# Kernel tuning notes

Hardware: AMD Instinct MI355X
Metric: run time of the kernel (lower is better)

## Reference

```python
import jax, jax.numpy as jnp
import numpy as np

# Production-scale dims: ViT patch attention on a 32x32 patch grid
B, L, F = 16, 1024, 512      # batch, seq (=NX*NY patches), model dim
H, D = 8, 64                 # heads, head_dim (F = H*D)
NX, NY = 32, 32              # patch grid; Toeplitz table size 4*NX*NY = 4096


def setup_inputs() -> dict:
    key = jax.random.key(0)
    ks = jax.random.split(key, 12)
    w = lambda k, shp: jax.random.normal(k, shp, jnp.float32) * 0.02
    return {
        "inputs_q": jax.random.normal(ks[0], (B, L, F), jnp.float32),
        "inputs_kv": jax.random.normal(ks[1], (B, L, F), jnp.float32),
        "Wq": w(ks[2], (F, H * D)), "bq": jnp.zeros((H * D,), jnp.float32),
        "Wk": w(ks[3], (F, H * D)), "bk": jnp.zeros((H * D,), jnp.float32),
        "Wv": w(ks[4], (F, H * D)), "bv": jnp.zeros((H * D,), jnp.float32),
        "Wo": w(ks[5], (H * D, F)), "bo": jnp.zeros((F,), jnp.float32),
        "toeplitz": w(ks[6], (H, 4 * NX * NY)),
    }


def _rel_index():
    # 2D relative-position (Toeplitz) index: patch p -> (x, y) on NX x NY grid.
    coords = jnp.arange(L)
    xi, yi = coords // NY, coords % NY
    dx = xi[:, None] - xi[None, :] + NX          # in [1, 2*NX-1]
    dy = yi[:, None] - yi[None, :] + NY          # in [1, 2*NY-1]
    return dx * (2 * NY) + dy                    # [L, L] indices into 4*NX*NY table


def reference(inputs_q, inputs_kv, Wq, bq, Wk, bk, Wv, bv, Wo, bo, toeplitz):
    q = (inputs_q @ Wq + bq).reshape(B, L, H, D)
    k = (inputs_kv @ Wk + bk).reshape(B, L, H, D)
    v = (inputs_kv @ Wv + bv).reshape(B, L, H, D)
    bias = toeplitz[:, _rel_index()]             # [H, L, L] Toeplitz relative bias
    scale = 1.0 / jnp.sqrt(jnp.float32(D))
    scores = jnp.einsum("bqhd,bkhd->bhqk", q, k) * scale + bias  # [B,H,L,L]
    attn = jax.nn.softmax(scores, axis=-1)
    x = jnp.einsum("bhqk,bkhd->bqhd", attn, v).reshape(B, L, H * D)
    out = x @ Wo + bo
    return out.reshape(B, L, H, D)               # matches torch forward's final reshape
```

## Files before the change

### kernel.cpp

```cpp
#include <hip/hip_runtime.h>
#include <hip/hip_bf16.h>

#define B_  16
#define L_  1024
#define F_  512
#define H_  8
#define D_  64
#define M_  (B_ * L_)
#define HD_ 512

typedef __bf16 bf16x8 __attribute__((ext_vector_type(8)));
typedef __bf16 bf16x4 __attribute__((ext_vector_type(4)));
typedef short  s16x4  __attribute__((ext_vector_type(4)));
typedef float  f32x4  __attribute__((ext_vector_type(4)));

__device__ __forceinline__ void gl_lds16(const void* g, void* l) {
  __builtin_amdgcn_global_load_lds(
      (const __attribute__((address_space(1))) unsigned int*)g,
      (__attribute__((address_space(3))) unsigned int*)l, 16, 0, 0);
}

__device__ __forceinline__ float exp2_fast(float x) {
  float r;
  asm("v_exp_f32 %0, %1" : "=v"(r) : "v"(x));
  return r;
}

#define WAIT_VM_LG(N)                                                           \
  asm volatile("s_waitcnt vmcnt(" #N ") lgkmcnt(0)" ::: "memory")
#define BARRIER() asm volatile("s_barrier" ::: "memory")

#define QSCALE 0.18033688f
#define LOG2E  1.44269504f

__global__ __launch_bounds__(256) void wt_kernel(
    const float* __restrict__ Wq, const float* __restrict__ Wk,
    const float* __restrict__ Wv, const float* __restrict__ Wo,
    __bf16* __restrict__ Wt_all)
{
  const float* W = (blockIdx.z == 0) ? Wq : (blockIdx.z == 1) ? Wk
                 : (blockIdx.z == 2) ? Wv : Wo;
  __bf16* Wt = Wt_all + (size_t)blockIdx.z * (512 * 512);
  __shared__ float s[32][33];
  const int t = threadIdx.x;
  const int r = t >> 5, c = t & 31;
  const int k0 = blockIdx.x * 32, n0 = blockIdx.y * 32;
#pragma unroll
  for (int i = 0; i < 4; ++i)
    s[r + i * 8][c] = W[(size_t)(k0 + r + i * 8) * 512 + n0 + c];
  __syncthreads();
#pragma unroll
  for (int i = 0; i < 4; ++i)
    Wt[(size_t)(n0 + r + i * 8) * 512 + k0 + c] = (__bf16)s[c][r + i * 8];
}

__global__ __launch_bounds__(256) void gemm_proj_kernel(
    const float* __restrict__ Xq, const float* __restrict__ Xkv,
    const __bf16* __restrict__ Wt_all,
    const float* __restrict__ bq, const float* __restrict__ bk_,
    const float* __restrict__ bv_,
    __bf16* __restrict__ qd, __bf16* __restrict__ kd, __bf16* __restrict__ vd)
{
  const int by = blockIdx.y;
  const int seg = by >> 2;
  const float* X = (seg == 0) ? Xq : Xkv;
  const __bf16* Wt = Wt_all + (size_t)seg * 262144;
  const float* bias = (seg == 0) ? bq : (seg == 1) ? bk_ : bv_;
  __bf16* dst = (seg == 0) ? qd : (seg == 1) ? kd : vd;
  const int mode = seg;
  const float oscale = (seg == 0) ? QSCALE : 1.0f;

  __shared__ __align__(16) __bf16 As[2][4][128][8];
  __shared__ __align__(16) __bf16 Bs[3][4][128][8];
  const int t = threadIdx.x;
  const int m0 = blockIdx.x * 128, n0 = (by & 3) * 128;
  const int lane = t & 63, w = t >> 6;
  const int ml = lane & 15, quad = lane >> 4;
  const int wm = w & 1, wn = w >> 1;

  f32x4 acc[4][4];
#pragma unroll
  for (int i = 0; i < 4; ++i)
#pragma unroll
    for (int j = 0; j < 4; ++j) acc[i][j] = (f32x4){0.f, 0.f, 0.f, 0.f};

  const int ako0 = t & 3,          arow0 = t >> 2;
  const int ako1 = (t + 256) & 3,  arow1 = (t + 256) >> 2;
  const int bs0 = w * 64 + lane,   bs1 = (w + 4) * 64 + lane;
  const int bko0 = bs0 >> 7, brow0 = bs0 & 127;
  const int bko1 = bs1 >> 7, brow1 = bs1 & 127;

  float4 fa0, fa1, fa2, fa3;

#define ALOAD(kk)                                                               \
  do {                                                                          \
    const float* p0 = X + (size_t)(m0 + arow0) * 512 + (kk) + ako0 * 8;         \
    const float* p1 = X + (size_t)(m0 + arow1) * 512 + (kk) + ako1 * 8;         \
    fa0 = *(const float4*)p0; fa1 = *(const float4*)(p0 + 4);                   \
    fa2 = *(const float4*)p1; fa3 = *(const float4*)(p1 + 4);                   \
  } while (0)

#define AWRITE(buf)                                                             \
  do {                                                                          \
    bf16x8 v0, v1;                                                              \
    v0[0] = (__bf16)fa0.x; v0[1] = (__bf16)fa0.y; v0[2] = (__bf16)fa0.z;        \
    v0[3] = (__bf16)fa0.w; v0[4] = (__bf16)fa1.x; v0[5] = (__bf16)fa1.y;        \
    v0[6] = (__bf16)fa1.z; v0[7] = (__bf16)fa1.w;                               \
    v1[0] = (__bf16)fa2.x; v1[1] = (__bf16)fa2.y; v1[2] = (__bf16)fa2.z;        \
    v1[3] = (__bf16)fa2.w; v1[4] = (__bf16)fa3.x; v1[5] = (__bf16)fa3.y;        \
    v1[6] = (__bf16)fa3.z; v1[7] = (__bf16)fa3.w;                               \
    *(bf16x8*)&As[buf][ako0][arow0][0] = v0;                                    \
    *(bf16x8*)&As[buf][ako1][arow1][0] = v1;                                    \
  } while (0)

#define BSTAGE(buf, kk)                                                         \
  do {                                                                          \
    gl_lds16(&Wt[(size_t)(n0 + brow0) * 512 + (kk) + bko0 * 8],                 \
             &Bs[buf][bko0][brow0][0]);                                         \
    gl_lds16(&Wt[(size_t)(n0 + brow1) * 512 + (kk) + bko1 * 8],                 \
             &Bs[buf][bko1][brow1][0]);                                         \
  } while (0)

#define COMPUTE_TILE(ab, bb)                                                    \
  do {                                                                          \
    bf16x8 a[4], b[4];                                                          \
    _Pragma("unroll") for (int mt = 0; mt < 4; ++mt)                            \
        a[mt] = *(const bf16x8*)&As[ab][quad][wm * 64 + mt * 16 + ml][0];       \
    _Pragma("unroll") for (int nt = 0; nt < 4; ++nt)                            \
        b[nt] = *(const bf16x8*)&Bs[bb][quad][wn * 64 + nt * 16 + ml][0];       \
    _Pragma("unroll") for (int mt = 0; mt < 4; ++mt)                            \
        _Pragma("unroll") for (int nt = 0; nt < 4; ++nt)                        \
            acc[mt][nt] = __builtin_amdgcn_mfma_f32_16x16x32_bf16(              \
                a[mt], b[nt], acc[mt][nt], 0, 0, 0);                            \
  } while (0)

  ALOAD(0);
  BSTAGE(0, 0);
  BSTAGE(1, 32);
  AWRITE(0);
  WAIT_VM_LG(2);
  BARRIER();

  int bcur = 0, bst = 2;
  for (int tt = 0; tt < 16; ++tt) {
    if (tt < 15) ALOAD((tt + 1) * 32);
    if (tt < 14) BSTAGE(bst, (tt + 2) * 32);
    COMPUTE_TILE(tt & 1, bcur);
    if (tt < 14) {
      WAIT_VM_LG(2);
      AWRITE((tt + 1) & 1);
      asm volatile("s_waitcnt lgkmcnt(0)" ::: "memory");
      BARRIER();
    } else if (tt == 14) {
      WAIT_VM_LG(0);
      AWRITE((tt + 1) & 1);
      asm volatile("s_waitcnt lgkmcnt(0)" ::: "memory");
      BARRIER();
    }
    bcur = (bcur == 2) ? 0 : bcur + 1;
    bst = (bst == 2) ? 0 : bst + 1;
  }

#pragma unroll
  for (int nt = 0; nt < 4; ++nt) {
    int col = n0 + wn * 64 + nt * 16 + ml;
    float bv = bias[col];
    int h = col >> 6, d = col & 63;
#pragma unroll
    for (int mt = 0; mt < 4; ++mt) {
      int row0 = m0 + wm * 64 + mt * 16 + quad * 4;
      int bz = row0 >> 10;
      int l0 = row0 & 1023;
      if (mode == 2) {
        bf16x4 pk;
#pragma unroll
        for (int r = 0; r < 4; ++r) pk[r] = (__bf16)(acc[mt][nt][r] + bv);
        size_t idx = ((size_t)(bz * H_ + h) * D_ + d) * L_ + l0;
        *(bf16x4*)&dst[idx] = pk;
      } else {
        size_t base = ((size_t)(bz * H_ + h) * L_ + l0) * D_ + d;
#pragma unroll
        for (int r = 0; r < 4; ++r)
          dst[base + (size_t)r * D_] = (__bf16)((acc[mt][nt][r] + bv) * oscale);
      }
    }
  }
#undef ALOAD
#undef AWRITE
#undef BSTAGE
#undef COMPUTE_TILE
}

__global__ __launch_bounds__(256, 2) void attn_kernel(
    const __bf16* __restrict__ qg,
    const __bf16* __restrict__ kg,
    const __bf16* __restrict__ vg,
    const float* __restrict__ toep_g,
    __bf16* __restrict__ xg)
{
  __shared__ float toep[4096];
  __shared__ __align__(16) __bf16 Ks[2][64][64];
  __shared__ __align__(16) __bf16 Vs[2][64][64];

  const int t = threadIdx.x;
  const int n = blockIdx.x;
  const int bh = ((n >> 5) << 3) | (n & 7);
  const int q0 = ((n >> 3) & 3) * 256;
  const int h = bh & 7;
  const int lane = t & 63, w = t >> 6;
  const int ml = lane & 15, quad = lane >> 4;
  const int lo3 = lane >> 3;
  const int kop = lane & 7;

  const size_t qkbase = (size_t)bh * (L_ * D_);
  const size_t vbase  = (size_t)bh * (D_ * L_);

  {
    const float4* src = (const float4*)(toep_g + (size_t)h * 4096);
    float4* dl = (float4*)toep;
    for (int i = t; i < 1024; i += 256) {
      float4 v = src[i];
      v.x *= LOG2E; v.y *= LOG2E; v.z *= LOG2E; v.w *= LOG2E;
      dl[i] = v;
    }
  }

#pragma unroll
  for (int i = 0; i < 2; ++i) {
    int row = (w * 2 + i) * 8 + lo3;
    int ko = kop ^ lo3;
    gl_lds16(&kg[qkbase + (size_t)row * D_ + ko * 8], &Ks[0][row][kop * 8]);
    gl_lds16(&vg[vbase + (size_t)row * L_ + ko * 8], &Vs[0][row][kop * 8]);
  }

  bf16x8 qf[4][2];
#pragma unroll
  for (int qn = 0; qn < 4; ++qn) {
    const __bf16* qp =
        qg + qkbase + (size_t)(q0 + w * 64 + qn * 16 + ml) * D_ + quad * 8;
    qf[qn][0] = *(const bf16x8*)qp;
    qf[qn][1] = *(const bf16x8*)(qp + 32);
  }

  const s16x4 ones = {(short)0x3F80, (short)0x3F80, (short)0x3F80, (short)0x3F80};

  f32x4 acc_l[4];
  f32x4 o[4][4];
#pragma unroll
  for (int qn = 0; qn < 4; ++qn) {
    acc_l[qn] = (f32x4){0.f, 0.f, 0.f, 0.f};
#pragma unroll
    for (int dt = 0; dt < 4; ++dt) o[qn][dt] = (f32x4){0.f, 0.f, 0.f, 0.f};
  }

  __syncthreads();

  int cur = 0;
  for (int k0 = 0; k0 < L_; k0 += 64) {
    if (k0 + 64 < L_) {
      int nb = cur ^ 1;
#pragma unroll
      for (int i = 0; i < 2; ++i) {
        int row = (w * 2 + i) * 8 + lo3;
        int ko = kop ^ lo3;
        gl_lds16(&kg[qkbase + (size_t)(k0 + 64 + row) * D_ + ko * 8],
                 &Ks[nb][row][kop * 8]);
        gl_lds16(&vg[vbase + (size_t)row * L_ + k0 + 64 + ko * 8],
                 &Vs[nb][row][kop * 8]);
      }
    }

    const int cb0 = (((q0 + w * 64) >> 5) - (k0 >> 5) + 31) * 64 +
                    (ml - quad * 4 + 16);
    float tc[3][3][4];
#pragma unroll
    for (int a = 0; a < 3; ++a)
#pragma unroll
      for (int b = 0; b < 3; ++b) {
        const int cb = cb0 + a * 64 + b * 16;
#pragma unroll
        for (int r = 0; r < 4; ++r) tc[a][b][r] = toep[cb - r];
      }

#pragma unroll
    for (int nt = 0; nt < 4; ++nt) {
      bf16x8 kf0 = *(const bf16x8*)&Ks[cur][nt * 16 + ml][(quad ^ (ml & 7)) * 8];
      bf16x8 kf1 =
          *(const bf16x8*)&Ks[cur][nt * 16 + ml][((4 + quad) ^ (ml & 7)) * 8];

      s16x4 pfrag[4];
#pragma unroll
      for (int qn = 0; qn < 4; ++qn) {
        f32x4 z = (f32x4){0.f, 0.f, 0.f, 0.f};
        z = __builtin_amdgcn_mfma_f32_16x16x32_bf16(kf0, qf[qn][0], z, 0, 0, 0);
        z = __builtin_amdgcn_mfma_f32_16x16x32_bf16(kf1, qf[qn][1], z, 0, 0, 0);

        float p[4];
#pragma unroll
        for (int r = 0; r < 4; ++r)
          p[r] = exp2_fast(z[r] + tc[(qn >> 1) - (nt >> 1) + 1]
                                    [(qn & 1) - (nt & 1) + 1][r]);
        bf16x4 pk;
#pragma unroll
        for (int r = 0; r < 4; ++r) pk[r] = (__bf16)p[r];
        pfrag[qn] = __builtin_bit_cast(s16x4, pk);
        acc_l[qn] = __builtin_amdgcn_mfma_f32_16x16x16bf16_1k(
            pfrag[qn], ones, acc_l[qn], 0, 0, 0);
      }

#pragma unroll
      for (int dt = 0; dt < 4; ++dt) {
        int row = dt * 16 + ml;
        int gc = nt * 2 + (quad >> 1);
        bf16x4 vfr = *(const bf16x4*)
            &Vs[cur][row][((gc ^ (row & 7)) * 8) + (quad & 1) * 4];
        s16x4 vfs = __builtin_bit_cast(s16x4, vfr);
#pragma unroll
        for (int qn = 0; qn < 4; ++qn)
          o[qn][dt] = __builtin_amdgcn_mfma_f32_16x16x16bf16_1k(
              pfrag[qn], vfs, o[qn][dt], 0, 0, 0);
      }
    }

    __syncthreads();
    cur ^= 1;
  }

  float linv[4][4];
#pragma unroll
  for (int qn = 0; qn < 4; ++qn)
#pragma unroll
    for (int r = 0; r < 4; ++r)
      linv[qn][r] = 1.0f / acc_l[qn][r];

#pragma unroll
  for (int qn = 0; qn < 4; ++qn)
#pragma unroll
    for (int dt = 0; dt < 4; ++dt)
#pragma unroll
      for (int r = 0; r < 4; ++r) {
        int row = q0 + w * 64 + qn * 16 + quad * 4 + r;
        xg[((size_t)(bh >> 3) * L_ + row) * 512 + h * 64 + dt * 16 + ml] =
            (__bf16)(o[qn][dt][r] * linv[qn][r]);
      }
}

__global__ __launch_bounds__(256, 2) void gemm_out_kernel(
    const __bf16* __restrict__ Xb,
    const __bf16* __restrict__ Wt,
    const float* __restrict__ bo,
    float* __restrict__ out)
{
  __shared__ __align__(16) __bf16 As[3][4][128][8];
  __shared__ __align__(16) __bf16 Bs[3][4][128][8];
  const int t = threadIdx.x;
  const int m0 = blockIdx.x * 128, n0 = blockIdx.y * 128;
  const int lane = t & 63, w = t >> 6;
  const int ml = lane & 15, quad = lane >> 4;
  const int wm = w & 1, wn = w >> 1;

  f32x4 acc[4][4];
#pragma unroll
  for (int i = 0; i < 4; ++i)
#pragma unroll
    for (int j = 0; j < 4; ++j) acc[i][j] = (f32x4){0.f, 0.f, 0.f, 0.f};

  const int slot0 = w * 64 + lane;
  const int slot1 = (w + 4) * 64 + lane;
  const int ko0 = slot0 >> 7, row0_ = slot0 & 127;
  const int ko1 = slot1 >> 7, row1_ = slot1 & 127;

#define STAGE_OUT(buf, kk)                                                      \
  do {                                                                          \
    gl_lds16(&Xb[(size_t)(m0 + row0_) * 512 + (kk) + ko0 * 8],                  \
             &As[buf][ko0][row0_][0]);                                          \
    gl_lds16(&Wt[(size_t)(n0 + row0_) * 512 + (kk) + ko0 * 8],                  \
             &Bs[buf][ko0][row0_][0]);                                          \
    gl_lds16(&Xb[(size_t)(m0 + row1_) * 512 + (kk) + ko1 * 8],                  \
             &As[buf][ko1][row1_][0]);                                          \
    gl_lds16(&Wt[(size_t)(n0 + row1_) * 512 + (kk) + ko1 * 8],                  \
             &Bs[buf][ko1][row1_][0]);                                          \
  } while (0)

#define COMPUTE_TILE_O(buf)                                                     \
  do {                                                                          \
    bf16x8 a[4], b[4];                                                          \
    _Pragma("unroll") for (int mt = 0; mt < 4; ++mt)                            \
        a[mt] = *(const bf16x8*)&As[buf][quad][wm * 64 + mt * 16 + ml][0];      \
    _Pragma("unroll") for (int nt = 0; nt < 4; ++nt)                            \
        b[nt] = *(const bf16x8*)&Bs[buf][quad][wn * 64 + nt * 16 + ml][0];      \
    _Pragma("unroll") for (int mt = 0; mt < 4; ++mt)                            \
        _Pragma("unroll") for (int nt = 0; nt < 4; ++nt)                        \
            acc[mt][nt] = __builtin_amdgcn_mfma_f32_16x16x32_bf16(              \
                a[mt], b[nt], acc[mt][nt], 0, 0, 0);                            \
  } while (0)

  STAGE_OUT(0, 0);
  STAGE_OUT(1, 32);

  int bcur = 0, bst = 2;
  for (int tt = 0; tt < 15; ++tt) {
    WAIT_VM_LG(4);
    BARRIER();
    if (tt < 14) STAGE_OUT(bst, (tt + 2) * 32);
    COMPUTE_TILE_O(bcur);
    bcur = (bcur == 2) ? 0 : bcur + 1;
    bst = (bst == 2) ? 0 : bst + 1;
  }
  WAIT_VM_LG(0);
  BARRIER();
  COMPUTE_TILE_O(bcur);

#pragma unroll
  for (int nt = 0; nt < 4; ++nt) {
    int col = n0 + wn * 64 + nt * 16 + ml;
    float bv = bo[col];
#pragma unroll
    for (int mt = 0; mt < 4; ++mt) {
      int row0 = m0 + wm * 64 + mt * 16 + quad * 4;
#pragma unroll
      for (int r = 0; r < 4; ++r)
        out[(size_t)(row0 + r) * 512 + col] = acc[mt][nt][r] + bv;
    }
  }
#undef STAGE_OUT
#undef COMPUTE_TILE_O
}

extern "C" void kernel_launch(void* const* d_in, const int* in_sizes, int n_in,
                              void* d_out, int out_size, void* d_ws, size_t ws_size,
                              hipStream_t stream) {
  const float* inputs_q  = (const float*)d_in[0];
  const float* inputs_kv = (const float*)d_in[1];
  const float* Wq = (const float*)d_in[2];
  const float* bq = (const float*)d_in[3];
  const float* Wk = (const float*)d_in[4];
  const float* bk = (const float*)d_in[5];
  const float* Wv = (const float*)d_in[6];
  const float* bv = (const float*)d_in[7];
  const float* Wo = (const float*)d_in[8];
  const float* bo = (const float*)d_in[9];
  const float* toep = (const float*)d_in[10];
  float* out = (float*)d_out;

  char* ws = (char*)d_ws;
  __bf16* qb  = (__bf16*)(ws);
  __bf16* kb  = (__bf16*)(ws + 16777216);
  __bf16* vb  = (__bf16*)(ws + 33554432);
  __bf16* xb  = (__bf16*)(ws + 50331648);
  __bf16* Wt  = (__bf16*)(ws + 67108864);

  wt_kernel<<<dim3(16, 16, 4), 256, 0, stream>>>(Wq, Wk, Wv, Wo, Wt);
  gemm_proj_kernel<<<dim3(128, 12), 256, 0, stream>>>(
      inputs_q, inputs_kv, Wt, bq, bk, bv, qb, kb, vb);
  attn_kernel<<<dim3(512), 256, 0, stream>>>(qb, kb, vb, toep, xb);
  gemm_out_kernel<<<dim3(128, 4), 256, 0, stream>>>(xb, Wt + 3 * 262144, bo, out);
}
```

Measured before the change: 258.5 us.

## Enlarge projection GEMM tile to 256x128 with 512 threads and grouped block order

The QKV projection GEMM now uses 512-thread blocks computing 256x128 output tiles, so each staged weight tile is shared by twice as many rows. Blocks are launched on a 1D grid remapped so that groups of 8 row-blocks sweep all 12 column tiles together, which is meant to improve L2 reuse of the fp32 activations. Each thread now issues a single LDS-direct load per B stage, and the wait counts are adjusted to match. The larger LDS footprint and the 4-blocks-per-CU launch bound may limit occupancy or registers.

```diff
diff --git a/kernel.cpp b/kernel.cpp
--- a/kernel.cpp
+++ b/kernel.cpp
@@ -54,15 +54,20 @@
     Wt[(size_t)(n0 + r + i * 8) * 512 + k0 + c] = (__bf16)s[c][r + i * 8];
 }
 
-__global__ __launch_bounds__(256) void gemm_proj_kernel(
+__global__ __launch_bounds__(512, 4) void gemm_proj_kernel(
     const float* __restrict__ Xq, const float* __restrict__ Xkv,
     const __bf16* __restrict__ Wt_all,
     const float* __restrict__ bq, const float* __restrict__ bk_,
     const float* __restrict__ bv_,
     __bf16* __restrict__ qd, __bf16* __restrict__ kd, __bf16* __restrict__ vd)
 {
-  const int by = blockIdx.y;
-  const int seg = by >> 2;
+  const int n = blockIdx.x;
+  const int idx = n >> 3;
+  const int mg = (n & 7) + 8 * (idx / 12);
+  const int j = idx % 12;
+  const int seg = j >> 2;
+  const int m0 = mg * 256, n0 = (j & 3) * 128;
+
   const float* X = (seg == 0) ? Xq : Xkv;
   const __bf16* Wt = Wt_all + (size_t)seg * 262144;
   const float* bias = (seg == 0) ? bq : (seg == 1) ? bk_ : bv_;
@@ -70,34 +75,31 @@
   const int mode = seg;
   const float oscale = (seg == 0) ? QSCALE : 1.0f;
 
-  __shared__ __align__(16) __bf16 As[2][4][128][8];
+  __shared__ __align__(16) __bf16 As[2][4][256][8];
   __shared__ __align__(16) __bf16 Bs[3][4][128][8];
   const int t = threadIdx.x;
-  const int m0 = blockIdx.x * 128, n0 = (by & 3) * 128;
   const int lane = t & 63, w = t >> 6;
   const int ml = lane & 15, quad = lane >> 4;
-  const int wm = w & 1, wn = w >> 1;
+  const int wm = w & 3, wn = w >> 2;
 
   f32x4 acc[4][4];
 #pragma unroll
   for (int i = 0; i < 4; ++i)
 #pragma unroll
-    for (int j = 0; j < 4; ++j) acc[i][j] = (f32x4){0.f, 0.f, 0.f, 0.f};
-
-  const int ako0 = t & 3,          arow0 = t >> 2;
-  const int ako1 = (t + 256) & 3,  arow1 = (t + 256) >> 2;
-  const int bs0 = w * 64 + lane,   bs1 = (w + 4) * 64 + lane;
-  const int bko0 = bs0 >> 7, brow0 = bs0 & 127;
-  const int bko1 = bs1 >> 7, brow1 = bs1 & 127;
+    for (int jj = 0; jj < 4; ++jj) acc[i][jj] = (f32x4){0.f, 0.f, 0.f, 0.f};
+
+  const int akoA = t >> 8;
+  const int arow = t & 255;
+  const int bko = t >> 7;
+  const int brow = t & 127;
 
   float4 fa0, fa1, fa2, fa3;
 
 #define ALOAD(kk)                                                               \
   do {                                                                          \
-    const float* p0 = X + (size_t)(m0 + arow0) * 512 + (kk) + ako0 * 8;         \
-    const float* p1 = X + (size_t)(m0 + arow1) * 512 + (kk) + ako1 * 8;         \
-    fa0 = *(const float4*)p0; fa1 = *(const float4*)(p0 + 4);                   \
-    fa2 = *(const float4*)p1; fa3 = *(const float4*)(p1 + 4);                   \
+    const float* p = X + (size_t)(m0 + arow) * 512 + (kk) + akoA * 8;           \
+    fa0 = *(const float4*)p;        fa1 = *(const float4*)(p + 4);              \
+    fa2 = *(const float4*)(p + 16); fa3 = *(const float4*)(p + 20);             \
   } while (0)
 
 #define AWRITE(buf)                                                             \
@@ -109,17 +111,13 @@
     v1[0] = (__bf16)fa2.x; v1[1] = (__bf16)fa2.y; v1[2] = (__bf16)fa2.z;        \
     v1[3] = (__bf16)fa2.w; v1[4] = (__bf16)fa3.x; v1[5] = (__bf16)fa3.y;        \
     v1[6] = (__bf16)fa3.z; v1[7] = (__bf16)fa3.w;                               \
-    *(bf16x8*)&As[buf][ako0][arow0][0] = v0;                                    \
-    *(bf16x8*)&As[buf][ako1][arow1][0] = v1;                                    \
+    *(bf16x8*)&As[buf][akoA][arow][0] = v0;                                     \
+    *(bf16x8*)&As[buf][akoA + 2][arow][0] = v1;                                 \
   } while (0)
 
 #define BSTAGE(buf, kk)                                                         \
-  do {                                                                          \
-    gl_lds16(&Wt[(size_t)(n0 + brow0) * 512 + (kk) + bko0 * 8],                 \
-             &Bs[buf][bko0][brow0][0]);                                         \
-    gl_lds16(&Wt[(size_t)(n0 + brow1) * 512 + (kk) + bko1 * 8],                 \
-             &Bs[buf][bko1][brow1][0]);                                         \
-  } while (0)
+  gl_lds16(&Wt[(size_t)(n0 + brow) * 512 + (kk) + bko * 8],                     \
+           &Bs[buf][bko][brow][0])
 
 #define COMPUTE_TILE(ab, bb)                                                    \
   do {                                                                          \
@@ -138,7 +136,7 @@
   BSTAGE(0, 0);
   BSTAGE(1, 32);
   AWRITE(0);
-  WAIT_VM_LG(2);
+  WAIT_VM_LG(1);
   BARRIER();
 
   int bcur = 0, bst = 2;
@@ -146,15 +144,13 @@
     if (tt < 15) ALOAD((tt + 1) * 32);
     if (tt < 14) BSTAGE(bst, (tt + 2) * 32);
     COMPUTE_TILE(tt & 1, bcur);
-    if (tt < 14) {
-      WAIT_VM_LG(2);
+    if (tt < 15) {
       AWRITE((tt + 1) & 1);
-      asm volatile("s_waitcnt lgkmcnt(0)" ::: "memory");
-      BARRIER();
-    } else if (tt == 14) {
-      WAIT_VM_LG(0);
-      AWRITE((tt + 1) & 1);
-      asm volatile("s_waitcnt lgkmcnt(0)" ::: "memory");
+      if (tt < 14) {
+        WAIT_VM_LG(1);
+      } else {
+        WAIT_VM_LG(0);
+      }
       BARRIER();
     }
     bcur = (bcur == 2) ? 0 : bcur + 1;
@@ -175,8 +171,8 @@
         bf16x4 pk;
 #pragma unroll
         for (int r = 0; r < 4; ++r) pk[r] = (__bf16)(acc[mt][nt][r] + bv);
-        size_t idx = ((size_t)(bz * H_ + h) * D_ + d) * L_ + l0;
-        *(bf16x4*)&dst[idx] = pk;
+        size_t idxo = ((size_t)(bz * H_ + h) * D_ + d) * L_ + l0;
+        *(bf16x4*)&dst[idxo] = pk;
       } else {
         size_t base = ((size_t)(bz * H_ + h) * L_ + l0) * D_ + d;
 #pragma unroll
@@ -451,7 +447,7 @@
   __bf16* Wt  = (__bf16*)(ws + 67108864);
 
   wt_kernel<<<dim3(16, 16, 4), 256, 0, stream>>>(Wq, Wk, Wv, Wo, Wt);
-  gemm_proj_kernel<<<dim3(128, 12), 256, 0, stream>>>(
+  gemm_proj_kernel<<<dim3(768), 512, 0, stream>>>(
       inputs_q, inputs_kv, Wt, bq, bk, bv, qb, kb, vb);
   attn_kernel<<<dim3(512), 256, 0, stream>>>(qb, kb, vb, toep, xb);
   gemm_out_kernel<<<dim3(128, 4), 256, 0, stream>>>(xb, Wt + 3 * 262144, bo, out);
```

Result: slower. 278.1 us (+7.6%).
